# Optimization experiments

Hardware: AMD Instinct MI355X
Metric: run time of the kernel (lower is better)

Reference implementation:

```python
import jax, jax.numpy as jnp
import numpy as np

N_NODES = 50000
IN_C, HID_C, OUT_C = 128, 128, 64
N_EDGES = 800000


def setup_inputs() -> dict:
    key = jax.random.key(0)
    k1, k2, k3, k4, k5, k6 = jax.random.split(key, 6)
    x = jax.random.normal(k1, (N_NODES, IN_C), dtype=jnp.float32)
    edge_index = jax.random.randint(k2, (2, N_EDGES), 0, N_NODES, dtype=jnp.int64)
    # Glorot-ish init for the two GCN layer weights + biases
    W1 = jax.random.normal(k3, (IN_C, HID_C), dtype=jnp.float32) / np.sqrt(IN_C)
    b1 = jnp.zeros((HID_C,), dtype=jnp.float32)
    W2 = jax.random.normal(k4, (HID_C, OUT_C), dtype=jnp.float32) / np.sqrt(HID_C)
    b2 = jnp.zeros((OUT_C,), dtype=jnp.float32)
    return {"x": x, "edge_index": edge_index, "W1": W1, "b1": b1, "W2": W2, "b2": b2}


def _gcn_norm(edge_index, num_nodes):
    # Add self-loops, then symmetric normalization: deg^-1/2[row] * deg^-1/2[col]
    loops = jnp.arange(num_nodes, dtype=edge_index.dtype)
    row = jnp.concatenate([edge_index[0], loops])  # target nodes
    col = jnp.concatenate([edge_index[1], loops])  # source nodes
    ones = jnp.ones(row.shape[0], dtype=jnp.float32)
    deg = jax.ops.segment_sum(ones, row, num_segments=num_nodes)
    dinv = jnp.where(deg > 0, jax.lax.rsqrt(jnp.maximum(deg, 1.0)), 0.0)
    norm = dinv[row] * dinv[col]  # [E + N]
    return row, col, norm


def _gcn_conv(x, row, col, norm, W, b, num_nodes):
    h = x @ W                              # [N, C_out] — transform first (fewer FLOPs)
    msg = h[col] * norm[:, None]           # gather + scale  [E+N, C_out]
    out = jax.ops.segment_sum(msg, row, num_segments=num_nodes)  # scatter-add
    return out + b


def reference(x, edge_index, W1, b1, W2, b2):
    n = x.shape[0]
    row, col, norm = _gcn_norm(edge_index, n)
    h = _gcn_conv(x, row, col, norm, W1, b1, n)
    # original applies x.relu() then non_linearity (ReLU()) — idempotent, one relu suffices
    h = jax.nn.relu(h)
    return _gcn_conv(h, row, col, norm, W2, b2, n)
```

## Files before the change

### kernel.cpp

```cpp
#include <hip/hip_runtime.h>


#define CHUNKS 256
#define CAP    7168

typedef short bf16x8 __attribute__((ext_vector_type(8)));
typedef float f32x4 __attribute__((ext_vector_type(4)));

__device__ __forceinline__ float bf2f(unsigned int u16) {
    return __uint_as_float(u16 << 16);
}
__device__ __forceinline__ unsigned int f2bf_rne(float f) {
    unsigned int u = __float_as_uint(f);
    return (u + 0x7fffu + ((u >> 16) & 1u)) >> 16;
}
__device__ __forceinline__ unsigned int pack2bf(float a, float b) {
    return f2bf_rne(a) | (f2bf_rne(b) << 16);
}
__device__ __forceinline__ void add8(float* acc, uint4 p) {
    acc[0] += bf2f(p.x & 0xffffu); acc[1] += bf2f(p.x >> 16);
    acc[2] += bf2f(p.y & 0xffffu); acc[3] += bf2f(p.y >> 16);
    acc[4] += bf2f(p.z & 0xffffu); acc[5] += bf2f(p.z >> 16);
    acc[6] += bf2f(p.w & 0xffffu); acc[7] += bf2f(p.w >> 16);
}

__global__ __launch_bounds__(256) void p1_kernel(
    const int* __restrict__ row, const int* __restrict__ col, int E, int CE, int NB,
    const float* __restrict__ W1, const float* __restrict__ W2,
    unsigned short* __restrict__ Wt1, unsigned short* __restrict__ Wt2,
    int* __restrict__ pos, unsigned int* __restrict__ bucketc)
{
    __shared__ int hist[256], scn[256], cur[256];
    const int c = blockIdx.x, t = threadIdx.x;
    const int s = c * CE, e = min(E, s + CE);

    hist[t] = 0;
    __syncthreads();
    for (int i = s + t; i < e; i += 256) atomicAdd(&hist[row[i] >> 8], 1);
    {
        int i = c * 256 + t;
        if (i < 128 * 128) {
            int k = i >> 7, cc = i & 127;
            Wt1[cc * 128 + k] = (unsigned short)f2bf_rne(W1[i]);
        } else if (i < 128 * 128 + 128 * 64) {
            int j = i - 128 * 128;
            int k = j >> 6, cc = j & 63;
            Wt2[cc * 128 + k] = (unsigned short)f2bf_rne(W2[j]);
        }
    }
    __syncthreads();

    int v = hist[t];
    scn[t] = v;
    __syncthreads();
    #pragma unroll
    for (int d = 1; d < 256; d <<= 1) {
        int xv = (t >= d) ? scn[t - d] : 0;
        __syncthreads();
        scn[t] += xv;
        __syncthreads();
    }
    int excl = scn[t] - v;
    if (t <= NB) pos[t * CHUNKS + c] = excl;
    cur[t] = excl;
    __syncthreads();

    for (int i = s + t; i < e; i += 256) {
        int r = row[i];
        int p = atomicAdd(&cur[r >> 8], 1);
        bucketc[s + p] = (unsigned)(r & 255) | ((unsigned)col[i] << 8);
    }
}

__global__ __launch_bounds__(256) void p2_kernel(
    const int* __restrict__ pos, const unsigned int* __restrict__ bucketc,
    unsigned int* __restrict__ csrf, float* __restrict__ dinv,
    int4* __restrict__ nod, int N, int CE)
{
    __shared__ unsigned int ent[CAP];
    __shared__ int stmp[256], hist[256], scn[256], cnt2[256], smtot[1];
    const int b = blockIdx.x, t = threadIdx.x;

    const int p0 = pos[b * CHUNKS + t];
    const int p1 = pos[(b + 1) * CHUNKS + t];
    const int cnt = p1 - p0;

    stmp[t] = cnt;
    hist[t] = 0;
    cnt2[t] = 0;
    __syncthreads();
    #pragma unroll
    for (int d = 1; d < 256; d <<= 1) {
        int xv = (t >= d) ? stmp[t - d] : 0;
        __syncthreads();
        stmp[t] += xv;
        __syncthreads();
    }
    const int fbase = stmp[t] - cnt;
    if (t == 255) smtot[0] = stmp[255];
    __syncthreads();
    const int m = min(smtot[0], CAP);

    {
        const int src = t * CE + p0;
        int i = 0;
        for (; i + 1 < cnt; i += 2) {
            unsigned int u0 = bucketc[src + i];
            unsigned int u1 = bucketc[src + i + 1];
            int d0 = fbase + i;
            if (d0 + 1 < CAP) {
                ent[d0] = u0; ent[d0 + 1] = u1;
                atomicAdd(&hist[u0 & 255u], 1);
                atomicAdd(&hist[u1 & 255u], 1);
            }
        }
        if (i < cnt) {
            unsigned int u0 = bucketc[src + i];
            int d0 = fbase + i;
            if (d0 < CAP) {
                ent[d0] = u0;
                atomicAdd(&hist[u0 & 255u], 1);
            }
        }
    }
    __syncthreads();

    int h = hist[t];
    scn[t] = h;
    __syncthreads();
    #pragma unroll
    for (int d = 1; d < 256; d <<= 1) {
        int xv = (t >= d) ? scn[t - d] : 0;
        __syncthreads();
        scn[t] += xv;
        __syncthreads();
    }
    int base = scn[t] - h;

    int node = b * 256 + t;
    if (node < N) {
        float dv = rsqrtf((float)(h + 1));
        dinv[node] = dv;
        nod[node] = make_int4(b * CAP + base, b * CAP + base + h, __float_as_int(dv), 0);
    }
    scn[t] = base;
    __syncthreads();

    for (int i = t; i < m; i += 256) {
        unsigned int v = ent[i];
        int r = v & 255u;
        int slot = atomicAdd(&cnt2[r], 1);
        csrf[b * CAP + scn[r] + slot] = v >> 8;
    }
}

__global__ __launch_bounds__(256) void gemm_mfma_kernel(
    const float* __restrict__ X, const unsigned short* __restrict__ Wt,
    const float* __restrict__ dinv, unsigned short* __restrict__ out, int N)
{
    constexpr int COUT = 128;
    __shared__ unsigned short As[64 * 128];
    __shared__ unsigned short Bs[COUT * 128];
    __shared__ float dl[64];

    const int t = threadIdx.x;
    const int m0 = blockIdx.x * 64;

    #pragma unroll
    for (int i = 0; i < 8; ++i) {
        int f = i * 256 + t;
        int r = f >> 5, c4 = f & 31;
        int rg = m0 + r;
        float4 v = (rg < N) ? ((const float4*)X)[(size_t)rg * 32 + c4]
                            : make_float4(0.f, 0.f, 0.f, 0.f);
        uint2 p;
        p.x = pack2bf(v.x, v.y);
        p.y = pack2bf(v.z, v.w);
        int cb = c4 * 8;
        *(uint2*)((char*)As + r * 256 + (cb ^ ((r & 7) << 4))) = p;
    }
    #pragma unroll
    for (int i = 0; i < 16; ++i) {
        int f = i * 256 + t;
        int r = f >> 5;
        int cb = (f & 31) * 8;
        uint2 p = ((const uint2*)Wt)[f];
        *(uint2*)((char*)Bs + r * 256 + (cb ^ ((r & 7) << 4))) = p;
    }
    if (t < 64) dl[t] = (m0 + t < N) ? dinv[m0 + t] : 0.f;
    __syncthreads();

    const int w = t >> 6, l = t & 63;
    const int lr = l & 15, lk = l >> 4;

    bf16x8 af[4][4];
    #pragma unroll
    for (int mt = 0; mt < 4; ++mt)
        #pragma unroll
        for (int kt = 0; kt < 4; ++kt) {
            int r = mt * 16 + lr;
            int cb = kt * 64 + lk * 16;
            af[mt][kt] = *(const bf16x8*)((const char*)As + r * 256 + (cb ^ ((r & 7) << 4)));
        }
    bf16x8 bfr[2][4];
    #pragma unroll
    for (int ct = 0; ct < 2; ++ct)
        #pragma unroll
        for (int kt = 0; kt < 4; ++kt) {
            int c = w * 32 + ct * 16 + lr;
            int cb = kt * 64 + lk * 16;
            bfr[ct][kt] = *(const bf16x8*)((const char*)Bs + c * 256 + (cb ^ ((c & 7) << 4)));
        }

    f32x4 acc[4][2];
    #pragma unroll
    for (int mt = 0; mt < 4; ++mt)
        #pragma unroll
        for (int ct = 0; ct < 2; ++ct)
            acc[mt][ct] = f32x4{0.f, 0.f, 0.f, 0.f};

    #pragma unroll
    for (int kt = 0; kt < 4; ++kt)
        #pragma unroll
        for (int mt = 0; mt < 4; ++mt)
            #pragma unroll
            for (int ct = 0; ct < 2; ++ct)
                acc[mt][ct] = __builtin_amdgcn_mfma_f32_16x16x32_bf16(
                    af[mt][kt], bfr[ct][kt], acc[mt][ct], 0, 0, 0);

    #pragma unroll
    for (int mt = 0; mt < 4; ++mt) {
        #pragma unroll
        for (int ct = 0; ct < 2; ++ct) {
            #pragma unroll
            for (int r = 0; r < 4; ++r) {
                int rowl = mt * 16 + lk * 4 + r;
                int grow = m0 + rowl;
                if (grow < N) {
                    int c = w * 32 + ct * 16 + lr;
                    float v = acc[mt][ct][r] * dl[rowl];
                    out[(size_t)grow * COUT + c] = (unsigned short)f2bf_rne(v);
                }
            }
        }
    }
}

__global__ __launch_bounds__(1024) void agg1g2_kernel(
    const unsigned short* __restrict__ hs, const unsigned int* __restrict__ csr,
    const int4* __restrict__ nod, const float* __restrict__ bias ,
    const unsigned short* __restrict__ Wt2, unsigned short* __restrict__ hs2, int N)
{
    __shared__ unsigned short As[64 * 128];
    __shared__ unsigned short Bs[64 * 128];
    __shared__ float dl[64];

    const int t = threadIdx.x;
    const int w = t >> 6, l = t & 63;
    const int n0 = blockIdx.x * 64;
    const int sub = l >> 4, q = l & 15;
    const int rowl = w * 4 + sub;
    const int n = n0 + rowl;

    {
        int r = t >> 4;
        int cb = (t & 15) * 16;
        uint4 p = ((const uint4*)Wt2)[t];
        *(uint4*)((char*)Bs + r * 256 + (cb ^ ((r & 7) << 4))) = p;
    }

    float acc[8] = {};
    float dv = 0.f;
    if (n < N) {
        int4 se = nod[n];
        dv = __int_as_float(se.z);
        add8(acc, *(const uint4*)&hs[(size_t)n * 128 + q * 8]);
        int j = se.x;
        const int e = se.y;
        for (; j + 3 < e; j += 4) {
            int c0 = csr[j], c1 = csr[j + 1], c2 = csr[j + 2], c3 = csr[j + 3];
            uint4 p0 = *(const uint4*)&hs[(size_t)c0 * 128 + q * 8];
            uint4 p1 = *(const uint4*)&hs[(size_t)c1 * 128 + q * 8];
            uint4 p2 = *(const uint4*)&hs[(size_t)c2 * 128 + q * 8];
            uint4 p3 = *(const uint4*)&hs[(size_t)c3 * 128 + q * 8];
            add8(acc, p0);
            add8(acc, p1);
            add8(acc, p2);
            add8(acc, p3);
        }
        for (; j < e; ++j)
            add8(acc, *(const uint4*)&hs[(size_t)csr[j] * 128 + q * 8]);
    }

    {
        float4 b0 = ((const float4*)bias)[q * 2];
        float4 b1v = ((const float4*)bias)[q * 2 + 1];
        float v0 = fmaxf(dv * acc[0] + b0.x, 0.f), v1 = fmaxf(dv * acc[1] + b0.y, 0.f);
        float v2 = fmaxf(dv * acc[2] + b0.z, 0.f), v3 = fmaxf(dv * acc[3] + b0.w, 0.f);
        float v4 = fmaxf(dv * acc[4] + b1v.x, 0.f), v5 = fmaxf(dv * acc[5] + b1v.y, 0.f);
        float v6 = fmaxf(dv * acc[6] + b1v.z, 0.f), v7 = fmaxf(dv * acc[7] + b1v.w, 0.f);
        uint4 o;
        o.x = pack2bf(v0, v1); o.y = pack2bf(v2, v3);
        o.z = pack2bf(v4, v5); o.w = pack2bf(v6, v7);
        int cb = q * 16;
        *(uint4*)((char*)As + rowl * 256 + (cb ^ ((rowl & 7) << 4))) = o;
        if (q == 0) dl[rowl] = dv;
    }
    __syncthreads();

    const int lr = l & 15, lk = l >> 4;
    const int mt = w >> 2, ct = w & 3;

    bf16x8 af[4], bfr[4];
    #pragma unroll
    for (int kt = 0; kt < 4; ++kt) {
        int r = mt * 16 + lr;
        int cb = kt * 64 + lk * 16;
        af[kt] = *(const bf16x8*)((const char*)As + r * 256 + (cb ^ ((r & 7) << 4)));
        int c = ct * 16 + lr;
        bfr[kt] = *(const bf16x8*)((const char*)Bs + c * 256 + (cb ^ ((c & 7) << 4)));
    }
    f32x4 a = f32x4{0.f, 0.f, 0.f, 0.f};
    #pragma unroll
    for (int kt = 0; kt < 4; ++kt)
        a = __builtin_amdgcn_mfma_f32_16x16x32_bf16(af[kt], bfr[kt], a, 0, 0, 0);

    #pragma unroll
    for (int r = 0; r < 4; ++r) {
        int rowm = mt * 16 + lk * 4 + r;
        int grow = n0 + rowm;
        if (grow < N) {
            int c = ct * 16 + lr;
            float v = a[r] * dl[rowm];
            hs2[(size_t)grow * 64 + c] = (unsigned short)f2bf_rne(v);
        }
    }
}

__global__ __launch_bounds__(256) void agg2_kernel(
    const unsigned short* __restrict__ hs, const unsigned int* __restrict__ csr,
    const int4* __restrict__ nod, const float* __restrict__ bias,
    float* __restrict__ out, int N)
{
    const int w = threadIdx.x >> 6, l = threadIdx.x & 63;
    const int n = blockIdx.x * 4 + w;
    if (n >= N) return;
    const int q = l & 7, g = l >> 3;

    int4 se = nod[n];
    float acc[8] = {};
    if (g == 0)
        add8(acc, *(const uint4*)&hs[(size_t)n * 64 + q * 8]);

    int j = se.x + g;
    const int e = se.y;
    for (; j + 8 < e; j += 16) {
        int c0 = csr[j], c1 = csr[j + 8];
        uint4 p0 = *(const uint4*)&hs[(size_t)c0 * 64 + q * 8];
        uint4 p1 = *(const uint4*)&hs[(size_t)c1 * 64 + q * 8];
        add8(acc, p0);
        add8(acc, p1);
    }
    if (j < e)
        add8(acc, *(const uint4*)&hs[(size_t)csr[j] * 64 + q * 8]);

    #pragma unroll
    for (int i = 0; i < 8; ++i) {
        acc[i] += __shfl_xor(acc[i], 8);
        acc[i] += __shfl_xor(acc[i], 16);
        acc[i] += __shfl_xor(acc[i], 32);
    }

    if (g == 0) {
        float d = __int_as_float(se.z);
        float4 b0 = ((const float4*)bias)[q * 2];
        float4 b1 = ((const float4*)bias)[q * 2 + 1];
        float4 o0, o1;
        o0.x = d * acc[0] + b0.x; o0.y = d * acc[1] + b0.y;
        o0.z = d * acc[2] + b0.z; o0.w = d * acc[3] + b0.w;
        o1.x = d * acc[4] + b1.x; o1.y = d * acc[5] + b1.y;
        o1.z = d * acc[6] + b1.z; o1.w = d * acc[7] + b1.w;
        *(float4*)&out[(size_t)n * 64 + q * 8] = o0;
        *(float4*)&out[(size_t)n * 64 + q * 8 + 4] = o1;
    }
}

extern "C" void kernel_launch(void* const* d_in, const int* in_sizes, int n_in,
                              void* d_out, int out_size, void* d_ws, size_t ws_size,
                              hipStream_t stream)
{
    const float* x  = (const float*)d_in[0];
    const int*   ei = (const int*)d_in[1];
    const float* W1 = (const float*)d_in[2];
    const float* b1 = (const float*)d_in[3];
    const float* W2 = (const float*)d_in[4];
    const float* b2 = (const float*)d_in[5];
    float* out = (float*)d_out;

    const int N = in_sizes[0] / 128;
    const int E = in_sizes[1] / 2;
    const int* row = ei;
    const int* col = ei + E;
    const int NB = (N + 255) / 256;
    const int CE = (E + CHUNKS - 1) / CHUNKS;

    char* ws = (char*)d_ws;
    size_t o = 0;
    auto take = [&](size_t bytes) { void* p = ws + o; o = (o + bytes + 255) & ~(size_t)255; return p; };
    int*   pos    = (int*)  take((size_t)(NB + 1) * CHUNKS * 4);
    unsigned int* bucketc = (unsigned int*)take((size_t)E * 4);
    unsigned int* csrf    = (unsigned int*)take((size_t)NB * CAP * 4);
    float* dinv   = (float*)take((size_t)N * 4);
    int4*  nod    = (int4*) take((size_t)N * 16);
    unsigned short* Wt1 = (unsigned short*)take(128 * 128 * 2);
    unsigned short* Wt2 = (unsigned short*)take(64 * 128 * 2);
    unsigned short* hs  = (unsigned short*)take((size_t)N * 128 * 2);
    unsigned short* hs2 = (unsigned short*)take((size_t)N * 64 * 2);

    p1_kernel<<<CHUNKS, 256, 0, stream>>>(row, col, E, CE, NB, W1, W2, Wt1, Wt2,
                                          pos, bucketc);
    p2_kernel<<<NB, 256, 0, stream>>>(pos, bucketc, csrf, dinv, nod, N, CE);

    gemm_mfma_kernel<<<(N + 63) / 64, 256, 0, stream>>>(x, Wt1, dinv, hs, N);

    agg1g2_kernel<<<(N + 63) / 64, 1024, 0, stream>>>(hs, csrf, nod, b1, Wt2, hs2, N);

    agg2_kernel<<<(N + 3) / 4, 256, 0, stream>>>(hs2, csrf, nod, b2, out, N);
}
```

Baseline: 101.6 us.

## Balance edge aggregation across threads with per-block LDS atomic accumulation

The CSR entries now also pack the local row index (bits 17+) next to the source node. Both aggregation kernels split a 64-node block's edge range evenly across thread groups instead of assigning one node per group. Partial sums are flushed into a shared-memory fp32 tile with LDS atomics whenever the row changes. This targets load imbalance from skewed degrees, but adds LDS atomic traffic and a larger shared-memory footprint (32KB extra in agg1g2), which may lower occupancy.

```diff
diff --git a/kernel.cpp b/kernel.cpp
--- a/kernel.cpp
+++ b/kernel.cpp
@@ -22,6 +22,12 @@
     acc[2] += bf2f(p.y & 0xffffu); acc[3] += bf2f(p.y >> 16);
     acc[4] += bf2f(p.z & 0xffffu); acc[5] += bf2f(p.z >> 16);
     acc[6] += bf2f(p.w & 0xffffu); acc[7] += bf2f(p.w >> 16);
+}
+__device__ __forceinline__ void st8(float* dst, uint4 p) {
+    dst[0] = bf2f(p.x & 0xffffu); dst[1] = bf2f(p.x >> 16);
+    dst[2] = bf2f(p.y & 0xffffu); dst[3] = bf2f(p.y >> 16);
+    dst[4] = bf2f(p.z & 0xffffu); dst[5] = bf2f(p.z >> 16);
+    dst[6] = bf2f(p.w & 0xffffu); dst[7] = bf2f(p.w >> 16);
 }
 
 __global__ __launch_bounds__(256) void p1_kernel(
@@ -150,7 +156,7 @@
         unsigned int v = ent[i];
         int r = v & 255u;
         int slot = atomicAdd(&cnt2[r], 1);
-        csrf[b * CAP + scn[r] + slot] = v >> 8;
+        csrf[b * CAP + scn[r] + slot] = (v >> 8) | ((v & 255u) << 17);
     }
 }
 
@@ -251,15 +257,17 @@
     const int4* __restrict__ nod, const float* __restrict__ bias ,
     const unsigned short* __restrict__ Wt2, unsigned short* __restrict__ hs2, int N)
 {
+    __shared__ float Af[64][128];
     __shared__ unsigned short As[64 * 128];
     __shared__ unsigned short Bs[64 * 128];
     __shared__ float dl[64];
+    __shared__ int wse[2];
 
     const int t = threadIdx.x;
     const int w = t >> 6, l = t & 63;
     const int n0 = blockIdx.x * 64;
-    const int sub = l >> 4, q = l & 15;
-    const int rowl = w * 4 + sub;
+    const int q = l & 15;
+    const int rowl = t >> 4;
     const int n = n0 + rowl;
 
     {
@@ -268,43 +276,79 @@
         uint4 p = ((const uint4*)Wt2)[t];
         *(uint4*)((char*)Bs + r * 256 + (cb ^ ((r & 7) << 4))) = p;
     }
-
-    float acc[8] = {};
-    float dv = 0.f;
     if (n < N) {
-        int4 se = nod[n];
-        dv = __int_as_float(se.z);
-        add8(acc, *(const uint4*)&hs[(size_t)n * 128 + q * 8]);
-        int j = se.x;
-        const int e = se.y;
-        for (; j + 3 < e; j += 4) {
-            int c0 = csr[j], c1 = csr[j + 1], c2 = csr[j + 2], c3 = csr[j + 3];
-            uint4 p0 = *(const uint4*)&hs[(size_t)c0 * 128 + q * 8];
-            uint4 p1 = *(const uint4*)&hs[(size_t)c1 * 128 + q * 8];
-            uint4 p2 = *(const uint4*)&hs[(size_t)c2 * 128 + q * 8];
-            uint4 p3 = *(const uint4*)&hs[(size_t)c3 * 128 + q * 8];
+        uint4 sp = *(const uint4*)&hs[(size_t)n * 128 + q * 8];
+        st8(&Af[rowl][q * 8], sp);
+        if (q == 0) dl[rowl] = __int_as_float(nod[n].z);
+    } else {
+        #pragma unroll
+        for (int i = 0; i < 8; ++i) Af[rowl][q * 8 + i] = 0.f;
+        if (q == 0) dl[rowl] = 0.f;
+    }
+    if (t == 0) wse[0] = nod[n0].x;
+    if (t == 1) wse[1] = nod[min(n0 + 63, N - 1)].y;
+    __syncthreads();
+
+    {
+        const int w0 = wse[0], m = wse[1] - w0;
+        const int gid = (t >> 4);
+        int js = w0 + (gid * m) / 64;
+        int je = w0 + ((gid + 1) * m) / 64;
+        const int roff = n0 & 255;
+
+        float acc[8] = {};
+        int cur = -1;
+        #define FLUSH1() { if (cur >= 0) { \
+            atomicAdd(&Af[cur][q*8+0], acc[0]); atomicAdd(&Af[cur][q*8+1], acc[1]); \
+            atomicAdd(&Af[cur][q*8+2], acc[2]); atomicAdd(&Af[cur][q*8+3], acc[3]); \
+            atomicAdd(&Af[cur][q*8+4], acc[4]); atomicAdd(&Af[cur][q*8+5], acc[5]); \
+            atomicAdd(&Af[cur][q*8+6], acc[6]); atomicAdd(&Af[cur][q*8+7], acc[7]); \
+            acc[0]=0;acc[1]=0;acc[2]=0;acc[3]=0;acc[4]=0;acc[5]=0;acc[6]=0;acc[7]=0; } }
+
+        int j = js;
+        for (; j + 3 < je; j += 4) {
+            unsigned e0 = csr[j], e1 = csr[j + 1], e2 = csr[j + 2], e3 = csr[j + 3];
+            uint4 p0 = *(const uint4*)&hs[(size_t)(e0 & 0x1FFFFu) * 128 + q * 8];
+            uint4 p1 = *(const uint4*)&hs[(size_t)(e1 & 0x1FFFFu) * 128 + q * 8];
+            uint4 p2 = *(const uint4*)&hs[(size_t)(e2 & 0x1FFFFu) * 128 + q * 8];
+            uint4 p3 = *(const uint4*)&hs[(size_t)(e3 & 0x1FFFFu) * 128 + q * 8];
+            int r0 = (int)(e0 >> 17) - roff, r1 = (int)(e1 >> 17) - roff;
+            int r2 = (int)(e2 >> 17) - roff, r3 = (int)(e3 >> 17) - roff;
+            if (r0 != cur) { FLUSH1(); cur = r0; }
             add8(acc, p0);
+            if (r1 != cur) { FLUSH1(); cur = r1; }
             add8(acc, p1);
+            if (r2 != cur) { FLUSH1(); cur = r2; }
             add8(acc, p2);
+            if (r3 != cur) { FLUSH1(); cur = r3; }
             add8(acc, p3);
         }
-        for (; j < e; ++j)
-            add8(acc, *(const uint4*)&hs[(size_t)csr[j] * 128 + q * 8]);
-    }
+        for (; j < je; ++j) {
+            unsigned e0 = csr[j];
+            uint4 p0 = *(const uint4*)&hs[(size_t)(e0 & 0x1FFFFu) * 128 + q * 8];
+            int r0 = (int)(e0 >> 17) - roff;
+            if (r0 != cur) { FLUSH1(); cur = r0; }
+            add8(acc, p0);
+        }
+        FLUSH1();
+        #undef FLUSH1
+    }
+    __syncthreads();
 
     {
+        float d = dl[rowl];
         float4 b0 = ((const float4*)bias)[q * 2];
         float4 b1v = ((const float4*)bias)[q * 2 + 1];
-        float v0 = fmaxf(dv * acc[0] + b0.x, 0.f), v1 = fmaxf(dv * acc[1] + b0.y, 0.f);
-        float v2 = fmaxf(dv * acc[2] + b0.z, 0.f), v3 = fmaxf(dv * acc[3] + b0.w, 0.f);
-        float v4 = fmaxf(dv * acc[4] + b1v.x, 0.f), v5 = fmaxf(dv * acc[5] + b1v.y, 0.f);
-        float v6 = fmaxf(dv * acc[6] + b1v.z, 0.f), v7 = fmaxf(dv * acc[7] + b1v.w, 0.f);
+        const float* af = &Af[rowl][q * 8];
+        float v0 = fmaxf(d * af[0] + b0.x, 0.f), v1 = fmaxf(d * af[1] + b0.y, 0.f);
+        float v2 = fmaxf(d * af[2] + b0.z, 0.f), v3 = fmaxf(d * af[3] + b0.w, 0.f);
+        float v4 = fmaxf(d * af[4] + b1v.x, 0.f), v5 = fmaxf(d * af[5] + b1v.y, 0.f);
+        float v6 = fmaxf(d * af[6] + b1v.z, 0.f), v7 = fmaxf(d * af[7] + b1v.w, 0.f);
         uint4 o;
         o.x = pack2bf(v0, v1); o.y = pack2bf(v2, v3);
         o.z = pack2bf(v4, v5); o.w = pack2bf(v6, v7);
         int cb = q * 16;
         *(uint4*)((char*)As + rowl * 256 + (cb ^ ((rowl & 7) << 4))) = o;
-        if (q == 0) dl[rowl] = dv;
     }
     __syncthreads();
 
@@ -337,49 +381,90 @@
     }
 }
 
-__global__ __launch_bounds__(256) void agg2_kernel(
+__global__ __launch_bounds__(512) void agg2_kernel(
     const unsigned short* __restrict__ hs, const unsigned int* __restrict__ csr,
     const int4* __restrict__ nod, const float* __restrict__ bias,
     float* __restrict__ out, int N)
 {
-    const int w = threadIdx.x >> 6, l = threadIdx.x & 63;
-    const int n = blockIdx.x * 4 + w;
-    if (n >= N) return;
-    const int q = l & 7, g = l >> 3;
-
-    int4 se = nod[n];
-    float acc[8] = {};
-    if (g == 0)
-        add8(acc, *(const uint4*)&hs[(size_t)n * 64 + q * 8]);
-
-    int j = se.x + g;
-    const int e = se.y;
-    for (; j + 8 < e; j += 16) {
-        int c0 = csr[j], c1 = csr[j + 8];
-        uint4 p0 = *(const uint4*)&hs[(size_t)c0 * 64 + q * 8];
-        uint4 p1 = *(const uint4*)&hs[(size_t)c1 * 64 + q * 8];
-        add8(acc, p0);
-        add8(acc, p1);
-    }
-    if (j < e)
-        add8(acc, *(const uint4*)&hs[(size_t)csr[j] * 64 + q * 8]);
-
-    #pragma unroll
-    for (int i = 0; i < 8; ++i) {
-        acc[i] += __shfl_xor(acc[i], 8);
-        acc[i] += __shfl_xor(acc[i], 16);
-        acc[i] += __shfl_xor(acc[i], 32);
-    }
-
-    if (g == 0) {
-        float d = __int_as_float(se.z);
+    __shared__ float Bf[64][64];
+    __shared__ float dl[64];
+    __shared__ int wse[2];
+
+    const int t = threadIdx.x;
+    const int n0 = blockIdx.x * 64;
+    const int q = t & 7;
+    const int rowl = t >> 3;
+    const int n = n0 + rowl;
+
+    if (n < N) {
+        uint4 sp = *(const uint4*)&hs[(size_t)n * 64 + q * 8];
+        st8(&Bf[rowl][q * 8], sp);
+        if (q == 0) dl[rowl] = __int_as_float(nod[n].z);
+    } else {
+        #pragma unroll
+        for (int i = 0; i < 8; ++i) Bf[rowl][q * 8 + i] = 0.f;
+        if (q == 0) dl[rowl] = 0.f;
+    }
+    if (t == 0) wse[0] = nod[n0].x;
+    if (t == 1) wse[1] = nod[min(n0 + 63, N - 1)].y;
+    __syncthreads();
+
+    {
+        const int w0 = wse[0], m = wse[1] - w0;
+        const int gid = t >> 3;
+        int js = w0 + (gid * m) / 64;
+        int je = w0 + ((gid + 1) * m) / 64;
+        const int roff = n0 & 255;
+
+        float acc[8] = {};
+        int cur = -1;
+        #define FLUSH2() { if (cur >= 0) { \
+            atomicAdd(&Bf[cur][q*8+0], acc[0]); atomicAdd(&Bf[cur][q*8+1], acc[1]); \
+            atomicAdd(&Bf[cur][q*8+2], acc[2]); atomicAdd(&Bf[cur][q*8+3], acc[3]); \
+            atomicAdd(&Bf[cur][q*8+4], acc[4]); atomicAdd(&Bf[cur][q*8+5], acc[5]); \
+            atomicAdd(&Bf[cur][q*8+6], acc[6]); atomicAdd(&Bf[cur][q*8+7], acc[7]); \
+            acc[0]=0;acc[1]=0;acc[2]=0;acc[3]=0;acc[4]=0;acc[5]=0;acc[6]=0;acc[7]=0; } }
+
+        int j = js;
+        for (; j + 3 < je; j += 4) {
+            unsigned e0 = csr[j], e1 = csr[j + 1], e2 = csr[j + 2], e3 = csr[j + 3];
+            uint4 p0 = *(const uint4*)&hs[(size_t)(e0 & 0x1FFFFu) * 64 + q * 8];
+            uint4 p1 = *(const uint4*)&hs[(size_t)(e1 & 0x1FFFFu) * 64 + q * 8];
+            uint4 p2 = *(const uint4*)&hs[(size_t)(e2 & 0x1FFFFu) * 64 + q * 8];
+            uint4 p3 = *(const uint4*)&hs[(size_t)(e3 & 0x1FFFFu) * 64 + q * 8];
+            int r0 = (int)(e0 >> 17) - roff, r1 = (int)(e1 >> 17) - roff;
+            int r2 = (int)(e2 >> 17) - roff, r3 = (int)(e3 >> 17) - roff;
+            if (r0 != cur) { FLUSH2(); cur = r0; }
+            add8(acc, p0);
+            if (r1 != cur) { FLUSH2(); cur = r1; }
+            add8(acc, p1);
+            if (r2 != cur) { FLUSH2(); cur = r2; }
+            add8(acc, p2);
+            if (r3 != cur) { FLUSH2(); cur = r3; }
+            add8(acc, p3);
+        }
+        for (; j < je; ++j) {
+            unsigned e0 = csr[j];
+            uint4 p0 = *(const uint4*)&hs[(size_t)(e0 & 0x1FFFFu) * 64 + q * 8];
+            int r0 = (int)(e0 >> 17) - roff;
+            if (r0 != cur) { FLUSH2(); cur = r0; }
+            add8(acc, p0);
+        }
+        FLUSH2();
+        #undef FLUSH2
+    }
+    __syncthreads();
+
+    if (n < N) {
+        float d = dl[rowl];
         float4 b0 = ((const float4*)bias)[q * 2];
         float4 b1 = ((const float4*)bias)[q * 2 + 1];
+        const float* bf = &Bf[rowl][q * 8];
         float4 o0, o1;
-        o0.x = d * acc[0] + b0.x; o0.y = d * acc[1] + b0.y;
-        o0.z = d * acc[2] + b0.z; o0.w = d * acc[3] + b0.w;
-        o1.x = d * acc[4] + b1.x; o1.y = d * acc[5] + b1.y;
-        o1.z = d * acc[6] + b1.z; o1.w = d * acc[7] + b1.w;
+        o0.x = d * bf[0] + b0.x; o0.y = d * bf[1] + b0.y;
+        o0.z = d * bf[2] + b0.z; o0.w = d * bf[3] + b0.w;
+        o1.x = d * bf[4] + b1.x; o1.y = d * bf[5] + b1.y;
+        o1.z = d * bf[6] + b1.z; o1.w = d * bf[7] + b1.w;
         *(float4*)&out[(size_t)n * 64 + q * 8] = o0;
         *(float4*)&out[(size_t)n * 64 + q * 8 + 4] = o1;
     }
@@ -425,5 +510,5 @@
 
     agg1g2_kernel<<<(N + 63) / 64, 1024, 0, stream>>>(hs, csrf, nod, b1, Wt2, hs2, N);
 
-    agg2_kernel<<<(N + 3) / 4, 256, 0, stream>>>(hs2, csrf, nod, b2, out, N);
-}
+    agg2_kernel<<<(N + 63) / 64, 512, 0, stream>>>(hs2, csrf, nod, b2, out, N);
+}
```

Measured after the change: 184.4 us. 1.82x slower.
